# Kernel tuning notes

Measured on AMD Instinct MI355X. Metric: run time of the kernel, lower is better.

Reference implementation:

```python
import jax, jax.numpy as jnp
import numpy as np

LN_EPS = 1e-5

def layer_norm(x, g, b):
    m = x.mean(-1, keepdims=True)
    v = ((x - m) ** 2).mean(-1, keepdims=True)
    return (x - m) / jnp.sqrt(v + LN_EPS) * g + b

def gat_conv(x, src, dst, W, att_src, att_dst, bias, heads, out_ch, concat):
    # PyG GATConv (eval mode, self-loops already included in src/dst).
    N = x.shape[0]
    h = (x @ W).reshape(N, heads, out_ch)                 # [N,H,C]
    a_src = (h * att_src).sum(-1)                          # [N,H]
    a_dst = (h * att_dst).sum(-1)                          # [N,H]
    e = jax.nn.leaky_relu(a_src[src] + a_dst[dst], 0.2)   # [E,H]
    emax = jax.ops.segment_max(e, dst, num_segments=N)    # [N,H]
    ee = jnp.exp(e - emax[dst])
    denom = jax.ops.segment_sum(ee, dst, num_segments=N)  # [N,H]
    alpha = ee / (denom[dst] + 1e-16)                      # [E,H]
    out = jax.ops.segment_sum(alpha[:, :, None] * h[src], dst, num_segments=N)  # [N,H,C]
    out = out.reshape(N, heads * out_ch) if concat else out.mean(axis=1)
    return out + bias

def setup_inputs() -> dict:
    key = jax.random.key(0)
    ks = jax.random.split(key, 32)
    N, G, E = 50000, 405, 300000
    RH, GH, H = 256, 256, 4
    def w(k, shape, fan_in):
        return jax.random.normal(k, shape, dtype=jnp.float32) * (1.0 / np.sqrt(fan_in))
    d = {}
    d["x"] = jax.random.normal(ks[0], (N, G), dtype=jnp.float32)
    d["edge_index"] = jax.random.randint(ks[1], (2, E), 0, N, dtype=jnp.int64)
    # JointEncoder
    d["enc_w1"] = w(ks[2], (G, RH), G); d["enc_b1"] = jnp.zeros(RH)
    d["ln1_g"] = jnp.ones(RH); d["ln1_b"] = jnp.zeros(RH)
    d["enc_w2"] = w(ks[3], (RH, RH), RH); d["enc_b2"] = jnp.zeros(RH)
    d["ln2_g"] = jnp.ones(RH); d["ln2_b"] = jnp.zeros(RH)
    d["w1"] = w(ks[4], (RH, H * GH), RH)
    d["att_src1"] = w(ks[5], (H, GH), GH); d["att_dst1"] = w(ks[6], (H, GH), GH)
    d["bias1"] = jnp.zeros(H * GH)
    d["res1_w"] = w(ks[7], (RH, H * GH), RH); d["res1_b"] = jnp.zeros(H * GH)
    d["w2"] = w(ks[8], (H * GH, 2 * 96), H * GH)
    d["att_src2"] = w(ks[9], (2, 96), 96); d["att_dst2"] = w(ks[10], (2, 96), 96)
    d["bias2"] = jnp.zeros(2 * 96)
    d["res2_w"] = w(ks[11], (H * GH, 2 * 96), H * GH); d["res2_b"] = jnp.zeros(2 * 96)
    d["w3"] = w(ks[12], (192, 128), 192)
    d["att_src3"] = w(ks[13], (1, 128), 128); d["att_dst3"] = w(ks[14], (1, 128), 128)
    d["bias3"] = jnp.zeros(128)
    d["res3_w"] = w(ks[15], (192, 128), 192); d["res3_b"] = jnp.zeros(128)
    # MLP head
    d["mlp_w1"] = w(ks[16], (128, 64), 128); d["mlp_b1"] = jnp.zeros(64)
    d["mlp_w2"] = w(ks[17], (64, 2), 64); d["mlp_b2"] = jnp.zeros(2)
    return d

def reference(x, edge_index, enc_w1, enc_b1, ln1_g, ln1_b, enc_w2, enc_b2, ln2_g, ln2_b,
              w1, att_src1, att_dst1, bias1, res1_w, res1_b,
              w2, att_src2, att_dst2, bias2, res2_w, res2_b,
              w3, att_src3, att_dst3, bias3, res3_w, res3_b,
              mlp_w1, mlp_b1, mlp_w2, mlp_b2):
    N = x.shape[0]
    loop = jnp.arange(N, dtype=edge_index.dtype)
    src = jnp.concatenate([edge_index[0], loop])
    dst = jnp.concatenate([edge_index[1], loop])
    # JointEncoder (eval: dropout is identity)
    h = jax.nn.relu(layer_norm(x @ enc_w1 + enc_b1, ln1_g, ln1_b))
    h = jax.nn.relu(layer_norm(h @ enc_w2 + enc_b2, ln2_g, ln2_b))
    # Block 1
    idn = h
    h = jax.nn.elu(gat_conv(h, src, dst, w1, att_src1, att_dst1, bias1, 4, 256, True))
    h = h + (idn @ res1_w + res1_b)
    # Block 2
    idn = h
    h = jax.nn.elu(gat_conv(h, src, dst, w2, att_src2, att_dst2, bias2, 2, 96, True))
    h = h + (idn @ res2_w + res2_b)
    # Block 3
    idn = h
    h = jax.nn.elu(gat_conv(h, src, dst, w3, att_src3, att_dst3, bias3, 1, 128, False))
    h = h + (idn @ res3_w + res3_b)
    # MLP head
    out = jax.nn.relu(h @ mlp_w1 + mlp_b1) @ mlp_w2 + mlp_b2
    return out
```

## Files before the change

kernel.cpp:

```cpp
#include <hip/hip_runtime.h>
#include <cstddef>

#define LN_EPS 1e-5f

typedef __bf16 bf16x8 __attribute__((ext_vector_type(8)));
typedef float  f32x4  __attribute__((ext_vector_type(4)));

typedef __attribute__((address_space(3))) unsigned int lds_u32;
typedef __attribute__((address_space(1))) unsigned int glb_u32;

__device__ __forceinline__ void gl2lds16(const void* g, void* l) {
    __builtin_amdgcn_global_load_lds((const glb_u32*)g, (lds_u32*)l, 16, 0, 0);
}

__device__ __forceinline__ float b2f(ushort h) {
    return __uint_as_float(((unsigned)h) << 16);
}
__device__ __forceinline__ ushort f2b(float f) {
    unsigned u = __float_as_uint(f);
    return (ushort)((u + 0x7fffu + ((u >> 16) & 1u)) >> 16);
}
__device__ __forceinline__ unsigned pack2(float lo, float hi) {
    return (unsigned)f2b(lo) | ((unsigned)f2b(hi) << 16);
}
__device__ __forceinline__ uint2 pack4(const f32x4 v) {
    return make_uint2(pack2(v[0], v[1]), pack2(v[2], v[3]));
}

__device__ __forceinline__ void xcd_map(int& bx, int& by) {
    int NX = gridDim.x, MBr = gridDim.y;
    int L = blockIdx.y * NX + blockIdx.x;
    int G = NX * 8;
    int g = L / G;
    if (g * 8 + 8 <= MBr) {
        int r = L - g * G;
        by = g * 8 + (r & 7);
        bx = r >> 3;
    } else {
        by = L / NX;
        bx = L - by * NX;
    }
}

__device__ __forceinline__ float wave_allreduce_max(float v) {
    #pragma unroll
    for (int off = 32; off > 0; off >>= 1) v = fmaxf(v, __shfl_xor(v, off, 64));
    return v;
}
__device__ __forceinline__ float wave_allreduce_sum(float v) {
    #pragma unroll
    for (int off = 32; off > 0; off >>= 1) v += __shfl_xor(v, off, 64);
    return v;
}

__device__ __forceinline__ void stage3(const ushort* a0, const ushort* a1, const ushort* b0,
                                       ushort* __restrict__ As, ushort* __restrict__ Bs,
                                       int lb) {
    gl2lds16(a0, As + lb);
    gl2lds16(a1, As + lb + 4096);
    gl2lds16(b0, Bs + lb);
}

__device__ __forceinline__ void mfma_loop256(const ushort* aA0, const ushort* aA1,
                                             const ushort* aB0,
                                             ushort* __restrict__ As, ushort* __restrict__ Bs,
                                             int lb,
                                             int K, int wr, int wc, int cA, int l15,
                                             f32x4 acc[4][4]) {
    const int BUFA = 256 * 32;
    const int BUFB = 128 * 32;
    const int nk = K >> 5;
    stage3(aA0, aA1, aB0, As, Bs, lb);
    int p = 0;
    for (int t = 0; t < nk; t++) {
        asm volatile("s_waitcnt vmcnt(0)" ::: "memory");
        __builtin_amdgcn_s_barrier();
        __builtin_amdgcn_sched_barrier(0);
        int kn = (t + 1) * 32;
        if (kn < K) stage3(aA0 + kn, aA1 + kn, aB0 + kn,
                           As + (p ^ 1) * BUFA, Bs + (p ^ 1) * BUFB, lb);
        const ushort* Ac = As + p * BUFA;
        const ushort* Bc = Bs + p * BUFB;
        bf16x8 af[4], bf[4];
        #pragma unroll
        for (int i = 0; i < 4; i++)
            af[i] = *reinterpret_cast<const bf16x8*>(&Ac[(wr + i * 16 + l15) * 32 + cA]);
        #pragma unroll
        for (int j = 0; j < 4; j++)
            bf[j] = *reinterpret_cast<const bf16x8*>(&Bc[(wc + j * 16 + l15) * 32 + cA]);
        #pragma unroll
        for (int i = 0; i < 4; i++)
            #pragma unroll
            for (int j = 0; j < 4; j++)
                acc[i][j] = __builtin_amdgcn_mfma_f32_16x16x32_bf16(bf[j], af[i], acc[i][j], 0, 0, 0);
        p ^= 1;
    }
    __syncthreads();
}

template<int EPI>
__global__ __launch_bounds__(512, 4) void bgemm(const ushort* __restrict__ A,
                                                const ushort* __restrict__ BT,
                                                const float* __restrict__ bias,
                                                void* __restrict__ out, int ldc,
                                                float* __restrict__ Rf,
                                                float* __restrict__ Sf, int Fs,
                                                int M, int Ncols, int K, int lda) {
    __shared__ ushort As[2][256 * 32];
    __shared__ ushort Bs[2][128 * 32];
    const int tid = threadIdx.x;
    int bx, by; xcd_map(bx, by);
    const int m0 = by * 256, n0 = bx * 128;
    const int w = tid >> 6, lane = tid & 63;
    const int wr = (w >> 1) * 64, wc = (w & 1) * 64;
    const int quad = lane >> 4, l15 = lane & 15;
    const int cA = (quad ^ ((l15 >> 1) & 3)) * 8;
    const int lb = w * 512;

    const int r = tid >> 2, g = ((tid & 3) ^ ((tid >> 3) & 3)) * 8;
    int ga0 = m0 + r;       if (ga0 >= M) ga0 = M - 1;
    int ga1 = m0 + 128 + r; if (ga1 >= M) ga1 = M - 1;
    const ushort* aA0 = A + (size_t)ga0 * lda + g;
    const ushort* aA1 = A + (size_t)ga1 * lda + g;
    const ushort* aB0 = BT + (size_t)(n0 + r) * K + g;

    f32x4 acc[4][4] = {};
    mfma_loop256(aA0, aA1, aB0, As[0], Bs[0], lb, K, wr, wc, cA, l15, acc);

    if (EPI == 4) {
        if (wc == 0) {
            #pragma unroll
            for (int i = 0; i < 4; i++) {
                float o0 = 0.f, o1 = 0.f;
                #pragma unroll
                for (int j = 0; j < 4; j++) {
                    int colbase = j * 16 + quad * 4;
                    float4 bv = *reinterpret_cast<const float4*>(&bias[colbase]);
                    float bb[4] = { bv.x, bv.y, bv.z, bv.w };
                    #pragma unroll
                    for (int rr = 0; rr < 4; rr++) {
                        float vv = fmaxf(acc[i][j][rr] + bb[rr], 0.f);
                        int c = colbase + rr;
                        o0 += vv * Rf[2 * c];
                        o1 += vv * Rf[2 * c + 1];
                    }
                }
                o0 += __shfl_xor(o0, 16, 64); o0 += __shfl_xor(o0, 32, 64);
                o1 += __shfl_xor(o1, 16, 64); o1 += __shfl_xor(o1, 32, 64);
                int row = m0 + wr + i * 16 + l15;
                if (quad == 0 && row < M) {
                    ((float*)out)[(size_t)row * 2]     = o0 + Sf[0];
                    ((float*)out)[(size_t)row * 2 + 1] = o1 + Sf[1];
                }
            }
        }
        return;
    }

    const int twoH = Ncols - 2 * Fs;
    #pragma unroll
    for (int i = 0; i < 4; i++) {
        int row = m0 + wr + i * 16 + l15;
        if (row >= M) continue;
        #pragma unroll
        for (int j = 0; j < 4; j++) {
            int colbase = n0 + wc + j * 16 + quad * 4;
            if (EPI == 0) {
                f32x4 v = acc[i][j];
                if (bias) {
                    float4 bv = *reinterpret_cast<const float4*>(&bias[colbase]);
                    v[0] += bv.x; v[1] += bv.y; v[2] += bv.z; v[3] += bv.w;
                }
                *reinterpret_cast<f32x4*>(&((float*)out)[(size_t)row * ldc + colbase]) = v;
            } else if (EPI == 5) {
                if (colbase + 3 < Fs) {
                    *reinterpret_cast<uint2*>(&((ushort*)out)[(size_t)row * Fs + colbase]) = pack4(acc[i][j]);
                } else if (colbase >= Fs && colbase + 3 < 2 * Fs) {
                    *reinterpret_cast<f32x4*>(&Rf[(size_t)row * Fs + (colbase - Fs)]) = acc[i][j];
                } else {
                    #pragma unroll
                    for (int rr = 0; rr < 4; rr++) {
                        int col = colbase + rr;
                        if (col < 2 * Fs || col >= Ncols) continue;
                        Sf[(size_t)row * twoH + (col - 2 * Fs)] = acc[i][j][rr];
                    }
                }
            }
        }
    }
}

__global__ __launch_bounds__(512, 4) void bgemm_b1(const ushort* __restrict__ accb,
                                                   const ushort* __restrict__ w1T,
                                                   const ushort* __restrict__ h1b,
                                                   const ushort* __restrict__ res1T,
                                                   const float* __restrict__ bias1,
                                                   const float* __restrict__ res1b,
                                                   ushort* __restrict__ H2b, int M) {
    __shared__ ushort As[2][256 * 32];
    __shared__ ushort Bs[2][128 * 32];
    const int tid = threadIdx.x;
    int bx, by; xcd_map(bx, by);
    const int m0 = by * 256, n0 = bx * 128;
    const int h = n0 >> 8;
    const int w = tid >> 6, lane = tid & 63;
    const int wr = (w >> 1) * 64, wc = (w & 1) * 64;
    const int quad = lane >> 4, l15 = lane & 15;
    const int cA = (quad ^ ((l15 >> 1) & 3)) * 8;
    const int lb = w * 512;

    const int r = tid >> 2, g = ((tid & 3) ^ ((tid >> 3) & 3)) * 8;
    int ga0 = m0 + r;       if (ga0 >= M) ga0 = M - 1;
    int ga1 = m0 + 128 + r; if (ga1 >= M) ga1 = M - 1;

    f32x4 acc[4][4] = {};

    mfma_loop256(accb + (size_t)ga0 * 1024 + h * 256 + g,
                 accb + (size_t)ga1 * 1024 + h * 256 + g,
                 w1T + (size_t)(n0 + r) * 256 + g,
                 As[0], Bs[0], lb, 256, wr, wc, cA, l15, acc);

    #pragma unroll
    for (int i = 0; i < 4; i++) {
        #pragma unroll
        for (int j = 0; j < 4; j++) {
            int colbase = n0 + wc + j * 16 + quad * 4;
            float4 bv = *reinterpret_cast<const float4*>(&bias1[colbase]);
            float4 rv = *reinterpret_cast<const float4*>(&res1b[colbase]);
            float bb[4] = { bv.x, bv.y, bv.z, bv.w };
            float rr[4] = { rv.x, rv.y, rv.z, rv.w };
            #pragma unroll
            for (int q = 0; q < 4; q++) {
                float t = acc[i][j][q] + bb[q];
                t = t > 0.f ? t : (__expf(t) - 1.f);
                acc[i][j][q] = t + rr[q];
            }
        }
    }

    mfma_loop256(h1b + (size_t)ga0 * 256 + g,
                 h1b + (size_t)ga1 * 256 + g,
                 res1T + (size_t)(n0 + r) * 256 + g,
                 As[0], Bs[0], lb, 256, wr, wc, cA, l15, acc);

    #pragma unroll
    for (int i = 0; i < 4; i++) {
        int row = m0 + wr + i * 16 + l15;
        if (row >= M) continue;
        #pragma unroll
        for (int j = 0; j < 4; j++) {
            int colbase = n0 + wc + j * 16 + quad * 4;
            *reinterpret_cast<uint2*>(&H2b[(size_t)row * 1024 + colbase]) = pack4(acc[i][j]);
        }
    }
}

__global__ void conv_pad_x_kernel(const float* __restrict__ x, ushort* __restrict__ xb, int N) {
    int t = blockIdx.x * 256 + threadIdx.x;
    if (t >= N * 448) return;
    int n = t / 448, k = t - n * 448;
    xb[t] = f2b(k < 405 ? x[(size_t)n * 405 + k] : 0.f);
}

__device__ __forceinline__ void prep_seg(int t, const float* src, ushort* dst,
                                         int K, int Nreal, int Kpad, int ldsrc) {
    int n = t / Kpad, k = t - n * Kpad;
    float v = (k < K && n < Nreal) ? src[(size_t)k * ldsrc + n] : 0.f;
    dst[t] = f2b(v);
}

__global__ void prep_all_kernel(const float* __restrict__ enc_w1, const float* __restrict__ enc_w2,
                                const float* __restrict__ w1, const float* __restrict__ res1_w,
                                const float* __restrict__ w2, const float* __restrict__ res2_w,
                                const float* __restrict__ w3, const float* __restrict__ res3_w,
                                const float* __restrict__ mlp_w1,
                                ushort* __restrict__ enc_w1T, ushort* __restrict__ enc_w2T,
                                ushort* __restrict__ w1T, ushort* __restrict__ res1T,
                                ushort* __restrict__ Bcat2T, ushort* __restrict__ Bcat3T,
                                ushort* __restrict__ mlpw1T) {
    int t = blockIdx.x * 256 + threadIdx.x;
    const int c0 = 114688;
    const int c1 = c0 + 65536;
    const int c2 = c1 + 262144;
    const int c3 = c2 + 262144;
    const int c4 = c3 + 196608;
    const int c5 = c4 + 196608;
    const int c6 = c5 + 126976;
    const int c7 = c6 + 24576;
    const int c8 = c7 + 24576;
    const int c9 = c8 + 24192;
    const int c10 = c9 + 16384;
    if (t < c0)      prep_seg(t,        enc_w1, enc_w1T, 405, 256, 448, 256);
    else if (t < c1) prep_seg(t - c0,   enc_w2, enc_w2T, 256, 256, 256, 256);
    else if (t < c2) prep_seg(t - c1,   w1,     w1T,     256, 1024, 256, 1024);
    else if (t < c3) prep_seg(t - c2,   res1_w, res1T,   256, 1024, 256, 1024);
    else if (t < c4) prep_seg(t - c3,   w2,     Bcat2T,  1024, 192, 1024, 192);
    else if (t < c5) prep_seg(t - c4,   res2_w, Bcat2T + (size_t)192 * 1024, 1024, 192, 1024, 192);
    else if (t < c6) Bcat2T[(size_t)388 * 1024 + (t - c5)] = 0;
    else if (t < c7) prep_seg(t - c6,   w3,     Bcat3T,  192, 128, 192, 128);
    else if (t < c8) prep_seg(t - c7,   res3_w, Bcat3T + (size_t)128 * 192, 192, 128, 192, 128);
    else if (t < c9) Bcat3T[(size_t)258 * 192 + (t - c8)] = 0;
    else if (t < c10) prep_seg(t - c9,  mlp_w1, mlpw1T,  128, 64, 128, 64);
}

template<int H>
__global__ __launch_bounds__(256) void ln_relu_w_kernel(const float* __restrict__ x,
                                                        const float* __restrict__ g,
                                                        const float* __restrict__ b,
                                                        const float* __restrict__ qs,
                                                        const float* __restrict__ qd,
                                                        ushort* __restrict__ out,
                                                        float* __restrict__ a_s,
                                                        float* __restrict__ a_d,
                                                        int N) {
    const int lane = threadIdx.x & 63;
    int wid = blockIdx.x * 4 + (threadIdx.x >> 6);
    const int nw = gridDim.x * 4;
    const int c4 = lane * 4;

    f32x4 gv = *reinterpret_cast<const f32x4*>(&g[c4]);
    f32x4 bv = *reinterpret_cast<const f32x4*>(&b[c4]);
    f32x4 qsv[H > 0 ? H : 1], qdv[H > 0 ? H : 1];
    if (H > 0) {
        #pragma unroll
        for (int hh = 0; hh < H; hh++) {
            qsv[hh] = *reinterpret_cast<const f32x4*>(&qs[hh * 256 + c4]);
            qdv[hh] = *reinterpret_cast<const f32x4*>(&qd[hh * 256 + c4]);
        }
    }

    for (int row = wid; row < N; row += nw) {
        f32x4 v = *reinterpret_cast<const f32x4*>(&x[(size_t)row * 256 + c4]);
        float s  = v[0] + v[1] + v[2] + v[3];
        float s2 = v[0] * v[0] + v[1] * v[1] + v[2] * v[2] + v[3] * v[3];
        #pragma unroll
        for (int off = 32; off > 0; off >>= 1) {
            s  += __shfl_xor(s,  off, 64);
            s2 += __shfl_xor(s2, off, 64);
        }
        float m   = s * (1.f / 256.f);
        float var = s2 * (1.f / 256.f) - m * m;
        float rs  = rsqrtf(var + LN_EPS);
        f32x4 o;
        #pragma unroll
        for (int k = 0; k < 4; k++) o[k] = fmaxf((v[k] - m) * rs * gv[k] + bv[k], 0.f);
        *reinterpret_cast<uint2*>(&out[(size_t)row * 256 + c4]) =
            make_uint2(pack2(o[0], o[1]), pack2(o[2], o[3]));
        if (H > 0) {
            float sc[H > 0 ? 2 * H : 1];
            #pragma unroll
            for (int hh = 0; hh < H; hh++) {
                sc[hh]     = o[0] * qsv[hh][0] + o[1] * qsv[hh][1] + o[2] * qsv[hh][2] + o[3] * qsv[hh][3];
                sc[H + hh] = o[0] * qdv[hh][0] + o[1] * qdv[hh][1] + o[2] * qdv[hh][2] + o[3] * qdv[hh][3];
            }
            #pragma unroll
            for (int off = 32; off > 0; off >>= 1)
                #pragma unroll
                for (int k = 0; k < 2 * H; k++) sc[k] += __shfl_xor(sc[k], off, 64);
            if (lane == 0) {
                #pragma unroll
                for (int k = 0; k < H; k++) a_s[(size_t)row * H + k] = sc[k];
            } else if (lane == 1) {
                #pragma unroll
                for (int k = 0; k < H; k++) a_d[(size_t)row * H + k] = sc[H + k];
            }
        }
    }
}

__global__ void fold_att_kernel(const float* __restrict__ W,
                                const float* __restrict__ att_s,
                                const float* __restrict__ att_d,
                                float* __restrict__ qs, float* __restrict__ qd,
                                int Cin, int Cout, int H) {
    int t = blockIdx.x * blockDim.x + threadIdx.x;
    if (t >= H * Cin) return;
    int h = t / Cin, k = t - h * Cin;
    const float* wrow = W + (size_t)k * (H * Cout) + (size_t)h * Cout;
    const float* as = att_s + (size_t)h * Cout;
    const float* ad = att_d + (size_t)h * Cout;
    float ss = 0.f, sd = 0.f;
    for (int c = 0; c < Cout; c++) { float wv = wrow[c]; ss += wv * as[c]; sd += wv * ad[c]; }
    qs[t] = ss;
    qd[t] = sd;
}

__global__ void fold_att_b16_kernel(const float* __restrict__ W,
                                    const float* __restrict__ att_s,
                                    const float* __restrict__ att_d,
                                    ushort* __restrict__ qs_b, ushort* __restrict__ qd_b,
                                    int Cin, int Cout, int H) {
    int t = blockIdx.x * blockDim.x + threadIdx.x;
    if (t >= H * Cin) return;
    int h = t / Cin, k = t - h * Cin;
    const float* wrow = W + (size_t)k * (H * Cout) + (size_t)h * Cout;
    const float* as = att_s + (size_t)h * Cout;
    const float* ad = att_d + (size_t)h * Cout;
    float ss = 0.f, sd = 0.f;
    for (int c = 0; c < Cout; c++) { float wv = wrow[c]; ss += wv * as[c]; sd += wv * ad[c]; }
    qs_b[t] = f2b(ss);
    qd_b[t] = f2b(sd);
}

__device__ __forceinline__ void edge_sd(const int* ei, int e, int E, int& s, int& d) {
    if (e < E) { s = ei[e]; d = ei[E + e]; } else { s = d = e - E; }
}

__global__ void deg_kernel(const int* __restrict__ ei, int* __restrict__ deg, int E, int Et) {
    int e = blockIdx.x * blockDim.x + threadIdx.x;
    if (e >= Et) return;
    int s, d; edge_sd(ei, e, E, s, d);
    atomicAdd(&deg[d], 1);
}

__global__ __launch_bounds__(256) void scan1_kernel(const int* __restrict__ deg,
                                                    int* __restrict__ incl,
                                                    int* __restrict__ part, int N) {
    __shared__ int sd[256];
    int t = threadIdx.x;
    int i = blockIdx.x * 256 + t;
    int v = (i < N) ? deg[i] : 0;
    sd[t] = v; __syncthreads();
    #pragma unroll
    for (int o = 1; o < 256; o <<= 1) {
        int x = (t >= o) ? sd[t - o] : 0;
        __syncthreads();
        sd[t] += x;
        __syncthreads();
    }
    if (i < N) incl[i] = sd[t];
    if (t == 255) part[blockIdx.x] = sd[255];
}

__global__ __launch_bounds__(256) void scan2_kernel(int* __restrict__ part, int nb) {
    __shared__ int sd[256];
    int t = threadIdx.x;
    int v = (t < nb) ? part[t] : 0;
    sd[t] = v; __syncthreads();
    #pragma unroll
    for (int o = 1; o < 256; o <<= 1) {
        int x = (t >= o) ? sd[t - o] : 0;
        __syncthreads();
        sd[t] += x;
        __syncthreads();
    }
    if (t < nb) part[t] = sd[t];
}

__global__ void scan3_kernel(const int* __restrict__ incl, const int* __restrict__ deg,
                             const int* __restrict__ part, int* __restrict__ row_ptr, int N) {
    int i = blockIdx.x * blockDim.x + threadIdx.x;
    if (i >= N) return;
    int off = (blockIdx.x > 0) ? part[blockIdx.x - 1] : 0;
    row_ptr[i] = incl[i] - deg[i] + off;
}

__global__ void fill_kernel(const int* __restrict__ ei, const int* __restrict__ row_ptr,
                            int* __restrict__ cur, int* __restrict__ csr_src, int E, int Et) {
    int e = blockIdx.x * blockDim.x + threadIdx.x;
    if (e >= Et) return;
    int s, d; edge_sd(ei, e, E, s, d);
    int pos = row_ptr[d] + atomicAdd(&cur[d], 1);
    csr_src[pos] = s;
}

#define ACAP 256

__global__ __launch_bounds__(128) void aggr_b1_fused_kernel(const int* __restrict__ row_ptr,
                                                            const int* __restrict__ deg,
                                                            const int* __restrict__ csr_src,
                                                            const float* __restrict__ a_s,
                                                            const float* __restrict__ a_d,
                                                            const ushort* __restrict__ h1b,
                                                            ushort* __restrict__ accb) {
    __shared__ float alf[ACAP][4];
    __shared__ float sstat[8];
    int d = blockIdx.x, t = threadIdx.x;
    int base = row_ptr[d], dg = deg[d];
    float4 ad = *reinterpret_cast<const float4*>(&a_d[(size_t)d * 4]);
    if (t < 64) {
        float m0 = -1e30f, m1 = -1e30f, m2 = -1e30f, m3 = -1e30f;
        for (int j = t; j < dg; j += 64) {
            int s = csr_src[base + j];
            float4 sv = *reinterpret_cast<const float4*>(&a_s[(size_t)s * 4]);
            float c0 = sv.x + ad.x; c0 = c0 > 0.f ? c0 : 0.2f * c0; m0 = fmaxf(m0, c0);
            float c1 = sv.y + ad.y; c1 = c1 > 0.f ? c1 : 0.2f * c1; m1 = fmaxf(m1, c1);
            float c2 = sv.z + ad.z; c2 = c2 > 0.f ? c2 : 0.2f * c2; m2 = fmaxf(m2, c2);
            float c3 = sv.w + ad.w; c3 = c3 > 0.f ? c3 : 0.2f * c3; m3 = fmaxf(m3, c3);
        }
        m0 = wave_allreduce_max(m0); m1 = wave_allreduce_max(m1);
        m2 = wave_allreduce_max(m2); m3 = wave_allreduce_max(m3);
        float s0 = 0.f, s1 = 0.f, s2 = 0.f, s3 = 0.f;
        for (int j = t; j < dg; j += 64) {
            int s = csr_src[base + j];
            float4 sv = *reinterpret_cast<const float4*>(&a_s[(size_t)s * 4]);
            float c0 = sv.x + ad.x; c0 = c0 > 0.f ? c0 : 0.2f * c0; float e0 = __expf(c0 - m0); s0 += e0;
            float c1 = sv.y + ad.y; c1 = c1 > 0.f ? c1 : 0.2f * c1; float e1 = __expf(c1 - m1); s1 += e1;
            float c2 = sv.z + ad.z; c2 = c2 > 0.f ? c2 : 0.2f * c2; float e2 = __expf(c2 - m2); s2 += e2;
            float c3 = sv.w + ad.w; c3 = c3 > 0.f ? c3 : 0.2f * c3; float e3 = __expf(c3 - m3); s3 += e3;
            if (j < ACAP) { alf[j][0] = e0; alf[j][1] = e1; alf[j][2] = e2; alf[j][3] = e3; }
        }
        s0 = wave_allreduce_sum(s0); s1 = wave_allreduce_sum(s1);
        s2 = wave_allreduce_sum(s2); s3 = wave_allreduce_sum(s3);
        if (t == 0) {
            sstat[0] = m0; sstat[1] = m1; sstat[2] = m2; sstat[3] = m3;
            sstat[4] = 1.f / (s0 + 1e-16f); sstat[5] = 1.f / (s1 + 1e-16f);
            sstat[6] = 1.f / (s2 + 1e-16f); sstat[7] = 1.f / (s3 + 1e-16f);
        }
    }
    __syncthreads();
    float r0 = sstat[4], r1 = sstat[5], r2 = sstat[6], r3 = sstat[7];
    float a00 = 0, a01 = 0, a10 = 0, a11 = 0, a20 = 0, a21 = 0, a30 = 0, a31 = 0;
    for (int j = 0; j < dg; j++) {
        int s = csr_src[base + j];
        float al0, al1, al2, al3;
        if (j < ACAP) {
            al0 = alf[j][0] * r0; al1 = alf[j][1] * r1;
            al2 = alf[j][2] * r2; al3 = alf[j][3] * r3;
        } else {
            float4 sv = *reinterpret_cast<const float4*>(&a_s[(size_t)s * 4]);
            float c0 = sv.x + ad.x; c0 = c0 > 0.f ? c0 : 0.2f * c0; al0 = __expf(c0 - sstat[0]) * r0;
            float c1 = sv.y + ad.y; c1 = c1 > 0.f ? c1 : 0.2f * c1; al1 = __expf(c1 - sstat[1]) * r1;
            float c2 = sv.z + ad.z; c2 = c2 > 0.f ? c2 : 0.2f * c2; al2 = __expf(c2 - sstat[2]) * r2;
            float c3 = sv.w + ad.w; c3 = c3 > 0.f ? c3 : 0.2f * c3; al3 = __expf(c3 - sstat[3]) * r3;
        }
        unsigned v = reinterpret_cast<const unsigned*>(h1b + (size_t)s * 256)[t];
        float lo = b2f((ushort)(v & 0xffff)), hi = b2f((ushort)(v >> 16));
        a00 += al0 * lo; a01 += al0 * hi;
        a10 += al1 * lo; a11 += al1 * hi;
        a20 += al2 * lo; a21 += al2 * hi;
        a30 += al3 * lo; a31 += al3 * hi;
    }
    unsigned* o = reinterpret_cast<unsigned*>(accb + (size_t)d * 1024);
    o[t]       = pack2(a00, a01);
    o[t + 128] = pack2(a10, a11);
    o[t + 256] = pack2(a20, a21);
    o[t + 384] = pack2(a30, a31);
}

template<int H, int C, int F, int NT>
__global__ __launch_bounds__(NT) void aggr_comb_fused_kernel(const int* __restrict__ row_ptr,
                                                             const int* __restrict__ deg,
                                                             const int* __restrict__ csr_src,
                                                             const float* __restrict__ as,
                                                             const ushort* __restrict__ g,
                                                             const float* __restrict__ Rf,
                                                             const float* __restrict__ gb,
                                                             const float* __restrict__ rb,
                                                             ushort* __restrict__ outb) {
    __shared__ float alf[ACAP][H];
    __shared__ float sstat[2 * H];
    int d = blockIdx.x;
    int t = threadIdx.x;
    int base = row_ptr[d], dg = deg[d];
    if (t < 64) {
        float ad[H], mx[H];
        #pragma unroll
        for (int h = 0; h < H; h++) { ad[h] = as[(size_t)d * 2 * H + H + h]; mx[h] = -1e30f; }
        for (int j = t; j < dg; j += 64) {
            int s = csr_src[base + j];
            #pragma unroll
            for (int h = 0; h < H; h++) {
                float c = as[(size_t)s * 2 * H + h] + ad[h];
                c = c > 0.f ? c : 0.2f * c;
                mx[h] = fmaxf(mx[h], c);
            }
        }
        #pragma unroll
        for (int h = 0; h < H; h++) mx[h] = wave_allreduce_max(mx[h]);
        float sm[H];
        #pragma unroll
        for (int h = 0; h < H; h++) sm[h] = 0.f;
        for (int j = t; j < dg; j += 64) {
            int s = csr_src[base + j];
            #pragma unroll
            for (int h = 0; h < H; h++) {
                float c = as[(size_t)s * 2 * H + h] + ad[h];
                c = c > 0.f ? c : 0.2f * c;
                float e = __expf(c - mx[h]);
                sm[h] += e;
                if (j < ACAP) alf[j][h] = e;
            }
        }
        #pragma unroll
        for (int h = 0; h < H; h++) sm[h] = wave_allreduce_sum(sm[h]);
        if (t == 0) {
            #pragma unroll
            for (int h = 0; h < H; h++) { sstat[h] = mx[h]; sstat[H + h] = 1.f / (sm[h] + 1e-16f); }
        }
    }
    __syncthreads();
    int hd = (2 * t) / C;
    float mxv = sstat[hd], rdv = sstat[H + hd];
    float adv = as[(size_t)d * 2 * H + H + hd];
    float lo = 0.f, hi = 0.f;
    for (int j = 0; j < dg; j++) {
        int s = csr_src[base + j];
        float al;
        if (j < ACAP) al = alf[j][hd] * rdv;
        else {
            float c = as[(size_t)s * 2 * H + hd] + adv;
            c = c > 0.f ? c : 0.2f * c;
            al = __expf(c - mxv) * rdv;
        }
        unsigned v = reinterpret_cast<const unsigned*>(g + (size_t)s * F)[t];
        lo += al * b2f((ushort)(v & 0xffff));
        hi += al * b2f((ushort)(v >> 16));
    }
    int c0 = 2 * t, c1 = 2 * t + 1;
    float o0 = lo + gb[c0]; o0 = o0 > 0.f ? o0 : (__expf(o0) - 1.f);
    float o1 = hi + gb[c1]; o1 = o1 > 0.f ? o1 : (__expf(o1) - 1.f);
    o0 += Rf[(size_t)d * F + c0] + rb[c0];
    o1 += Rf[(size_t)d * F + c1] + rb[c1];
    reinterpret_cast<unsigned*>(outb)[(size_t)d * (F / 2) + t] = pack2(o0, o1);
}

extern "C" void kernel_launch(void* const* d_in, const int* in_sizes, int n_in,
                              void* d_out, int out_size, void* d_ws, size_t ws_size,
                              hipStream_t stream) {
    const float* x        = (const float*)d_in[0];
    const int*   ei       = (const int*)d_in[1];
    const float* enc_w1   = (const float*)d_in[2];
    const float* enc_b1   = (const float*)d_in[3];
    const float* ln1_g    = (const float*)d_in[4];
    const float* ln1_b    = (const float*)d_in[5];
    const float* enc_w2   = (const float*)d_in[6];
    const float* enc_b2   = (const float*)d_in[7];
    const float* ln2_g    = (const float*)d_in[8];
    const float* ln2_b    = (const float*)d_in[9];
    const float* w1       = (const float*)d_in[10];
    const float* att_src1 = (const float*)d_in[11];
    const float* att_dst1 = (const float*)d_in[12];
    const float* bias1    = (const float*)d_in[13];
    const float* res1_w   = (const float*)d_in[14];
    const float* res1_b   = (const float*)d_in[15];
    const float* w2       = (const float*)d_in[16];
    const float* att_src2 = (const float*)d_in[17];
    const float* att_dst2 = (const float*)d_in[18];
    const float* bias2    = (const float*)d_in[19];
    const float* res2_b_  = (const float*)d_in[21];
    const float* res2_w   = (const float*)d_in[20];
    const float* w3       = (const float*)d_in[22];
    const float* att_src3 = (const float*)d_in[23];
    const float* att_dst3 = (const float*)d_in[24];
    const float* bias3    = (const float*)d_in[25];
    const float* res3_w   = (const float*)d_in[26];
    const float* res3_b   = (const float*)d_in[27];
    const float* mlp_w1   = (const float*)d_in[28];
    const float* mlp_b1   = (const float*)d_in[29];
    const float* mlp_w2   = (const float*)d_in[30];
    const float* mlp_b2   = (const float*)d_in[31];
    const float* res2_b   = res2_b_;

    const int N  = in_sizes[0] / 405;
    const int E  = in_sizes[1] / 2;
    const int Et = E + N;
    const int NB = (N + 255) / 256;

    char* p = (char*)d_ws;
    char* R0 = p;
    char* R1 = R0 + (size_t)N * 896;
    char* R2 = R1 + (size_t)N * 512;
    char* R3 = R2 + (size_t)N * 512;
    char* R4 = R3 + (size_t)N * 2048;
    char* T  = R4 + (size_t)N * 2048;

    ushort* xb   = (ushort*)R0;
    ushort* H3b  = (ushort*)R0;
    ushort* h0b  = (ushort*)R1;
    ushort* G2b  = (ushort*)R1;
    ushort* h1b  = (ushort*)R2;
    ushort* G3b  = (ushort*)R2;
    ushort* H4b  = (ushort*)(R2 + (size_t)N * 256);
    float*  F1   = (float*)R3;
    ushort* H2b  = (ushort*)R3;
    ushort* accb = (ushort*)R4;
    float*  Rf   = (float*)R4;

    float* a_s   = (float*)T;                         T += (size_t)N * 4 * 4;
    float* a_d   = (float*)T;                         T += (size_t)N * 4 * 4;
    float* qs    = (float*)T;                         T += 2048 * 4;
    float* qd    = (float*)T;                         T += 2048 * 4;
    int* deg     = (int*)T;                           T += (size_t)N * 4;
    int* cur     = (int*)T;                           T += (size_t)N * 4;
    int* row_ptr = (int*)T;                           T += (size_t)N * 4;
    int* incl    = (int*)T;                           T += (size_t)N * 4;
    int* part    = (int*)T;                           T += 256 * 4;
    int* csr_src = (int*)T;                           T += (size_t)Et * 4;
    ushort* enc_w1T = (ushort*)T;                     T += (size_t)256 * 448 * 2;
    ushort* enc_w2T = (ushort*)T;                     T += (size_t)256 * 256 * 2;
    ushort* w1T     = (ushort*)T;                     T += (size_t)1024 * 256 * 2;
    ushort* res1T   = (ushort*)T;                     T += (size_t)1024 * 256 * 2;
    ushort* Bcat2T  = (ushort*)T;                     T += (size_t)512 * 1024 * 2;
    ushort* Bcat3T  = (ushort*)T;                     T += (size_t)384 * 192 * 2;
    ushort* mlpw1T  = (ushort*)T;                     T += (size_t)128 * 128 * 2;

    auto cdiv = [](int a, int b) { return (a + b - 1) / b; };
    const int MBr = cdiv(N, 256);

    hipMemsetAsync(deg, 0, (size_t)N * 8, stream);
    deg_kernel<<<cdiv(Et, 256), 256, 0, stream>>>(ei, deg, E, Et);
    scan1_kernel<<<NB, 256, 0, stream>>>(deg, incl, part, N);
    scan2_kernel<<<1, 256, 0, stream>>>(part, NB);
    scan3_kernel<<<NB, 256, 0, stream>>>(incl, deg, part, row_ptr, N);
    fill_kernel<<<cdiv(Et, 256), 256, 0, stream>>>(ei, row_ptr, cur, csr_src, E, Et);

    prep_all_kernel<<<cdiv(1314432, 256), 256, 0, stream>>>(
        enc_w1, enc_w2, w1, res1_w, w2, res2_w, w3, res3_w, mlp_w1,
        enc_w1T, enc_w2T, w1T, res1T, Bcat2T, Bcat3T, mlpw1T);

    fold_att_kernel<<<cdiv(4 * 256, 256), 256, 0, stream>>>(w1, att_src1, att_dst1, qs, qd, 256, 256, 4);

    conv_pad_x_kernel<<<cdiv(N * 448, 256), 256, 0, stream>>>(x, xb, N);
    bgemm<0><<<dim3(2, MBr), 512, 0, stream>>>(xb, enc_w1T, enc_b1, F1, 256, nullptr, nullptr, 0, N, 256, 448, 448);
    ln_relu_w_kernel<0><<<1024, 256, 0, stream>>>(F1, ln1_g, ln1_b, nullptr, nullptr, h0b, nullptr, nullptr, N);
    bgemm<0><<<dim3(2, MBr), 512, 0, stream>>>(h0b, enc_w2T, enc_b2, F1, 256, nullptr, nullptr, 0, N, 256, 256, 256);
    ln_relu_w_kernel<4><<<1024, 256, 0, stream>>>(F1, ln2_g, ln2_b, qs, qd, h1b, a_s, a_d, N);

    aggr_b1_fused_kernel<<<N, 128, 0, stream>>>(row_ptr, deg, csr_src, a_s, a_d, h1b, accb);
    bgemm_b1<<<dim3(8, MBr), 512, 0, stream>>>(accb, w1T, h1b, res1T, bias1, res1_b, H2b, N);

    {
        fold_att_b16_kernel<<<cdiv(2 * 1024, 256), 256, 0, stream>>>(w2, att_src2, att_dst2,
            Bcat2T + (size_t)384 * 1024, Bcat2T + (size_t)386 * 1024, 1024, 96, 2);
        bgemm<5><<<dim3(4, MBr), 512, 0, stream>>>(H2b, Bcat2T, nullptr, G2b, 0, Rf, a_s, 192, N, 388, 1024, 1024);
        aggr_comb_fused_kernel<2, 96, 192, 96><<<N, 96, 0, stream>>>(row_ptr, deg, csr_src, a_s,
                                                                     G2b, Rf, bias2, res2_b, H3b);
    }

    {
        fold_att_b16_kernel<<<1, 256, 0, stream>>>(w3, att_src3, att_dst3,
            Bcat3T + (size_t)256 * 192, Bcat3T + (size_t)257 * 192, 192, 128, 1);
        bgemm<5><<<dim3(3, MBr), 512, 0, stream>>>(H3b, Bcat3T, nullptr, G3b, 0, Rf, a_s, 128, N, 258, 192, 192);
        aggr_comb_fused_kernel<1, 128, 128, 64><<<N, 64, 0, stream>>>(row_ptr, deg, csr_src, a_s,
                                                                      G3b, Rf, bias3, res3_b, H4b);
    }

    bgemm<4><<<dim3(1, MBr), 512, 0, stream>>>(H4b, mlpw1T, mlp_b1, d_out, 2,
                                               (float*)mlp_w2, (float*)mlp_b2, 0, N, 64, 128, 128);
}
```

Before: 803.1 us.

## Fuse attention folding into prep kernel, process two rows per wave, unroll aggregation

Merges the three attention-vector folding kernels into the weight-prep kernel, using wave-parallel reductions instead of serial per-thread loops, which removes launches and long serial dot products. The layer-norm kernel now handles two rows per wave iteration and its grid doubles, raising memory-level parallelism. The edge aggregation loops are unrolled by two so two gathered rows are loaded before their accumulations, hiding gather latency. It costs more registers and a more complex prep kernel.

After: 724.3 us. 9.8% less time.

```diff
diff --git a/kernel.cpp b/kernel.cpp
--- a/kernel.cpp
+++ b/kernel.cpp
@@ -262,6 +262,7 @@
     xb[t] = f2b(k < 405 ? x[(size_t)n * 405 + k] : 0.f);
 }
 
+#define PREP_PB 5135
 __device__ __forceinline__ void prep_seg(int t, const float* src, ushort* dst,
                                          int K, int Nreal, int Kpad, int ldsrc) {
     int n = t / Kpad, k = t - n * Kpad;
@@ -269,38 +270,93 @@
     dst[t] = f2b(v);
 }
 
-__global__ void prep_all_kernel(const float* __restrict__ enc_w1, const float* __restrict__ enc_w2,
-                                const float* __restrict__ w1, const float* __restrict__ res1_w,
-                                const float* __restrict__ w2, const float* __restrict__ res2_w,
-                                const float* __restrict__ w3, const float* __restrict__ res3_w,
-                                const float* __restrict__ mlp_w1,
-                                ushort* __restrict__ enc_w1T, ushort* __restrict__ enc_w2T,
-                                ushort* __restrict__ w1T, ushort* __restrict__ res1T,
-                                ushort* __restrict__ Bcat2T, ushort* __restrict__ Bcat3T,
-                                ushort* __restrict__ mlpw1T) {
-    int t = blockIdx.x * 256 + threadIdx.x;
-    const int c0 = 114688;
-    const int c1 = c0 + 65536;
-    const int c2 = c1 + 262144;
-    const int c3 = c2 + 262144;
-    const int c4 = c3 + 196608;
-    const int c5 = c4 + 196608;
-    const int c6 = c5 + 126976;
-    const int c7 = c6 + 24576;
-    const int c8 = c7 + 24576;
-    const int c9 = c8 + 24192;
-    const int c10 = c9 + 16384;
-    if (t < c0)      prep_seg(t,        enc_w1, enc_w1T, 405, 256, 448, 256);
-    else if (t < c1) prep_seg(t - c0,   enc_w2, enc_w2T, 256, 256, 256, 256);
-    else if (t < c2) prep_seg(t - c1,   w1,     w1T,     256, 1024, 256, 1024);
-    else if (t < c3) prep_seg(t - c2,   res1_w, res1T,   256, 1024, 256, 1024);
-    else if (t < c4) prep_seg(t - c3,   w2,     Bcat2T,  1024, 192, 1024, 192);
-    else if (t < c5) prep_seg(t - c4,   res2_w, Bcat2T + (size_t)192 * 1024, 1024, 192, 1024, 192);
-    else if (t < c6) Bcat2T[(size_t)388 * 1024 + (t - c5)] = 0;
-    else if (t < c7) prep_seg(t - c6,   w3,     Bcat3T,  192, 128, 192, 128);
-    else if (t < c8) prep_seg(t - c7,   res3_w, Bcat3T + (size_t)128 * 192, 192, 128, 192, 128);
-    else if (t < c9) Bcat3T[(size_t)258 * 192 + (t - c8)] = 0;
-    else if (t < c10) prep_seg(t - c9,  mlp_w1, mlpw1T,  128, 64, 128, 64);
+__global__ void prep_fold_kernel(const float* __restrict__ enc_w1, const float* __restrict__ enc_w2,
+                                 const float* __restrict__ w1, const float* __restrict__ res1_w,
+                                 const float* __restrict__ w2, const float* __restrict__ res2_w,
+                                 const float* __restrict__ w3, const float* __restrict__ res3_w,
+                                 const float* __restrict__ mlp_w1,
+                                 const float* __restrict__ att_s1, const float* __restrict__ att_d1,
+                                 const float* __restrict__ att_s2, const float* __restrict__ att_d2,
+                                 const float* __restrict__ att_s3, const float* __restrict__ att_d3,
+                                 ushort* __restrict__ enc_w1T, ushort* __restrict__ enc_w2T,
+                                 ushort* __restrict__ w1T, ushort* __restrict__ res1T,
+                                 ushort* __restrict__ Bcat2T, ushort* __restrict__ Bcat3T,
+                                 ushort* __restrict__ mlpw1T,
+                                 float* __restrict__ qs, float* __restrict__ qd) {
+    int blk = blockIdx.x;
+    if (blk < PREP_PB) {
+        int t = blk * 256 + threadIdx.x;
+        const int c0 = 114688;
+        const int c1 = c0 + 65536;
+        const int c2 = c1 + 262144;
+        const int c3 = c2 + 262144;
+        const int c4 = c3 + 196608;
+        const int c5 = c4 + 196608;
+        const int c6 = c5 + 126976;
+        const int c7 = c6 + 24576;
+        const int c8 = c7 + 24576;
+        const int c9 = c8 + 24192;
+        const int c10 = c9 + 16384;
+        if (t < c0)      prep_seg(t,        enc_w1, enc_w1T, 405, 256, 448, 256);
+        else if (t < c1) prep_seg(t - c0,   enc_w2, enc_w2T, 256, 256, 256, 256);
+        else if (t < c2) prep_seg(t - c1,   w1,     w1T,     256, 1024, 256, 1024);
+        else if (t < c3) prep_seg(t - c2,   res1_w, res1T,   256, 1024, 256, 1024);
+        else if (t < c4) prep_seg(t - c3,   w2,     Bcat2T,  1024, 192, 1024, 192);
+        else if (t < c5) prep_seg(t - c4,   res2_w, Bcat2T + (size_t)192 * 1024, 1024, 192, 1024, 192);
+        else if (t < c6) Bcat2T[(size_t)388 * 1024 + (t - c5)] = 0;
+        else if (t < c7) prep_seg(t - c6,   w3,     Bcat3T,  192, 128, 192, 128);
+        else if (t < c8) prep_seg(t - c7,   res3_w, Bcat3T + (size_t)128 * 192, 192, 128, 192, 128);
+        else if (t < c9) Bcat3T[(size_t)258 * 192 + (t - c8)] = 0;
+        else if (t < c10) prep_seg(t - c9,  mlp_w1, mlpw1T,  128, 64, 128, 64);
+        return;
+    }
+    int fw = (blk - PREP_PB) * 4 + (threadIdx.x >> 6);
+    int lane = threadIdx.x & 63;
+    if (fw < 1024) {
+        int h = fw >> 8, k = fw & 255;
+        const float* wrow = w1 + (size_t)k * 1024 + h * 256;
+        f32x4 wv = *reinterpret_cast<const f32x4*>(&wrow[lane * 4]);
+        f32x4 as = *reinterpret_cast<const f32x4*>(&att_s1[h * 256 + lane * 4]);
+        f32x4 ad = *reinterpret_cast<const f32x4*>(&att_d1[h * 256 + lane * 4]);
+        float ss = wv[0] * as[0] + wv[1] * as[1] + wv[2] * as[2] + wv[3] * as[3];
+        float sd = wv[0] * ad[0] + wv[1] * ad[1] + wv[2] * ad[2] + wv[3] * ad[3];
+        ss = wave_allreduce_sum(ss);
+        sd = wave_allreduce_sum(sd);
+        if (lane == 0) { qs[fw] = ss; qd[fw] = sd; }
+    } else if (fw < 1024 + 2048) {
+        int t = fw - 1024;
+        int h = t >> 10, k = t & 1023;
+        const float* wrow = w2 + (size_t)k * 192 + h * 96;
+        const float* as = att_s2 + h * 96;
+        const float* ad = att_d2 + h * 96;
+        float w0 = wrow[lane];
+        float ss = w0 * as[lane], sd = w0 * ad[lane];
+        if (lane < 32) {
+            float w1v = wrow[64 + lane];
+            ss += w1v * as[64 + lane];
+            sd += w1v * ad[64 + lane];
+        }
+        ss = wave_allreduce_sum(ss);
+        sd = wave_allreduce_sum(sd);
+        if (lane == 0) {
+            Bcat2T[(size_t)384 * 1024 + t] = f2b(ss);
+            Bcat2T[(size_t)386 * 1024 + t] = f2b(sd);
+        }
+    } else {
+        int t = fw - 3072;
+        if (t < 192) {
+            const float* wrow = w3 + (size_t)t * 128;
+            float w0 = wrow[lane], w1v = wrow[64 + lane];
+            float ss = w0 * att_s3[lane] + w1v * att_s3[64 + lane];
+            float sd = w0 * att_d3[lane] + w1v * att_d3[64 + lane];
+            ss = wave_allreduce_sum(ss);
+            sd = wave_allreduce_sum(sd);
+            if (lane == 0) {
+                Bcat3T[(size_t)256 * 192 + t] = f2b(ss);
+                Bcat3T[(size_t)257 * 192 + t] = f2b(sd);
+            }
+        }
+    }
 }
 
 template<int H>
@@ -329,77 +385,65 @@
         }
     }
 
-    for (int row = wid; row < N; row += nw) {
-        f32x4 v = *reinterpret_cast<const f32x4*>(&x[(size_t)row * 256 + c4]);
-        float s  = v[0] + v[1] + v[2] + v[3];
-        float s2 = v[0] * v[0] + v[1] * v[1] + v[2] * v[2] + v[3] * v[3];
+    for (int r0 = wid * 2; r0 < N; r0 += 2 * nw) {
+        int r1 = r0 + 1;
+        bool has1 = r1 < N;
+        f32x4 va = *reinterpret_cast<const f32x4*>(&x[(size_t)r0 * 256 + c4]);
+        f32x4 vb = has1 ? *reinterpret_cast<const f32x4*>(&x[(size_t)r1 * 256 + c4]) : va;
+        float sa  = va[0] + va[1] + va[2] + va[3];
+        float s2a = va[0] * va[0] + va[1] * va[1] + va[2] * va[2] + va[3] * va[3];
+        float sb  = vb[0] + vb[1] + vb[2] + vb[3];
+        float s2b = vb[0] * vb[0] + vb[1] * vb[1] + vb[2] * vb[2] + vb[3] * vb[3];
         #pragma unroll
         for (int off = 32; off > 0; off >>= 1) {
-            s  += __shfl_xor(s,  off, 64);
-            s2 += __shfl_xor(s2, off, 64);
-        }
-        float m   = s * (1.f / 256.f);
-        float var = s2 * (1.f / 256.f) - m * m;
-        float rs  = rsqrtf(var + LN_EPS);
-        f32x4 o;
-        #pragma unroll
-        for (int k = 0; k < 4; k++) o[k] = fmaxf((v[k] - m) * rs * gv[k] + bv[k], 0.f);
-        *reinterpret_cast<uint2*>(&out[(size_t)row * 256 + c4]) =
-            make_uint2(pack2(o[0], o[1]), pack2(o[2], o[3]));
+            sa  += __shfl_xor(sa,  off, 64);
+            sb  += __shfl_xor(sb,  off, 64);
+            s2a += __shfl_xor(s2a, off, 64);
+            s2b += __shfl_xor(s2b, off, 64);
+        }
+        float ma  = sa * (1.f / 256.f);
+        float mb  = sb * (1.f / 256.f);
+        float rsa = rsqrtf(s2a * (1.f / 256.f) - ma * ma + LN_EPS);
+        float rsb = rsqrtf(s2b * (1.f / 256.f) - mb * mb + LN_EPS);
+        f32x4 oa, ob;
+        #pragma unroll
+        for (int k = 0; k < 4; k++) {
+            oa[k] = fmaxf((va[k] - ma) * rsa * gv[k] + bv[k], 0.f);
+            ob[k] = fmaxf((vb[k] - mb) * rsb * gv[k] + bv[k], 0.f);
+        }
+        *reinterpret_cast<uint2*>(&out[(size_t)r0 * 256 + c4]) =
+            make_uint2(pack2(oa[0], oa[1]), pack2(oa[2], oa[3]));
+        if (has1)
+            *reinterpret_cast<uint2*>(&out[(size_t)r1 * 256 + c4]) =
+                make_uint2(pack2(ob[0], ob[1]), pack2(ob[2], ob[3]));
         if (H > 0) {
-            float sc[H > 0 ? 2 * H : 1];
+            float sc[H > 0 ? 4 * H : 1];
             #pragma unroll
             for (int hh = 0; hh < H; hh++) {
-                sc[hh]     = o[0] * qsv[hh][0] + o[1] * qsv[hh][1] + o[2] * qsv[hh][2] + o[3] * qsv[hh][3];
-                sc[H + hh] = o[0] * qdv[hh][0] + o[1] * qdv[hh][1] + o[2] * qdv[hh][2] + o[3] * qdv[hh][3];
+                sc[hh]           = oa[0] * qsv[hh][0] + oa[1] * qsv[hh][1] + oa[2] * qsv[hh][2] + oa[3] * qsv[hh][3];
+                sc[H + hh]       = oa[0] * qdv[hh][0] + oa[1] * qdv[hh][1] + oa[2] * qdv[hh][2] + oa[3] * qdv[hh][3];
+                sc[2 * H + hh]   = ob[0] * qsv[hh][0] + ob[1] * qsv[hh][1] + ob[2] * qsv[hh][2] + ob[3] * qsv[hh][3];
+                sc[3 * H + hh]   = ob[0] * qdv[hh][0] + ob[1] * qdv[hh][1] + ob[2] * qdv[hh][2] + ob[3] * qdv[hh][3];
             }
             #pragma unroll
             for (int off = 32; off > 0; off >>= 1)
                 #pragma unroll
-                for (int k = 0; k < 2 * H; k++) sc[k] += __shfl_xor(sc[k], off, 64);
+                for (int k = 0; k < 4 * H; k++) sc[k] += __shfl_xor(sc[k], off, 64);
             if (lane == 0) {
                 #pragma unroll
-                for (int k = 0; k < H; k++) a_s[(size_t)row * H + k] = sc[k];
+                for (int k = 0; k < H; k++) a_s[(size_t)r0 * H + k] = sc[k];
+                if (has1)
+                    #pragma unroll
+                    for (int k = 0; k < H; k++) a_s[(size_t)r1 * H + k] = sc[2 * H + k];
             } else if (lane == 1) {
                 #pragma unroll
-                for (int k = 0; k < H; k++) a_d[(size_t)row * H + k] = sc[H + k];
+                for (int k = 0; k < H; k++) a_d[(size_t)r0 * H + k] = sc[H + k];
+                if (has1)
+                    #pragma unroll
+                    for (int k = 0; k < H; k++) a_d[(size_t)r1 * H + k] = sc[3 * H + k];
             }
         }
     }
-}
-
-__global__ void fold_att_kernel(const float* __restrict__ W,
-                                const float* __restrict__ att_s,
-                                const float* __restrict__ att_d,
-                                float* __restrict__ qs, float* __restrict__ qd,
-                                int Cin, int Cout, int H) {
-    int t = blockIdx.x * blockDim.x + threadIdx.x;
-    if (t >= H * Cin) return;
-    int h = t / Cin, k = t - h * Cin;
-    const float* wrow = W + (size_t)k * (H * Cout) + (size_t)h * Cout;
-    const float* as = att_s + (size_t)h * Cout;
-    const float* ad = att_d + (size_t)h * Cout;
-    float ss = 0.f, sd = 0.f;
-    for (int c = 0; c < Cout; c++) { float wv = wrow[c]; ss += wv * as[c]; sd += wv * ad[c]; }
-    qs[t] = ss;
-    qd[t] = sd;
-}
-
-__global__ void fold_att_b16_kernel(const float* __restrict__ W,
-                                    const float* __restrict__ att_s,
-                                    const float* __restrict__ att_d,
-                                    ushort* __restrict__ qs_b, ushort* __restrict__ qd_b,
-                                    int Cin, int Cout, int H) {
-    int t = blockIdx.x * blockDim.x + threadIdx.x;
-    if (t >= H * Cin) return;
-    int h = t / Cin, k = t - h * Cin;
-    const float* wrow = W + (size_t)k * (H * Cout) + (size_t)h * Cout;
-    const float* as = att_s + (size_t)h * Cout;
-    const float* ad = att_d + (size_t)h * Cout;
-    float ss = 0.f, sd = 0.f;
-    for (int c = 0; c < Cout; c++) { float wv = wrow[c]; ss += wv * as[c]; sd += wv * ad[c]; }
-    qs_b[t] = f2b(ss);
-    qd_b[t] = f2b(sd);
 }
 
 __device__ __forceinline__ void edge_sd(const int* ei, int e, int E, int& s, int& d) {
@@ -511,9 +555,8 @@
     __syncthreads();
     float r0 = sstat[4], r1 = sstat[5], r2 = sstat[6], r3 = sstat[7];
     float a00 = 0, a01 = 0, a10 = 0, a11 = 0, a20 = 0, a21 = 0, a30 = 0, a31 = 0;
-    for (int j = 0; j < dg; j++) {
-        int s = csr_src[base + j];
-        float al0, al1, al2, al3;
+
+    auto alpha4 = [&](int j, int s, float& al0, float& al1, float& al2, float& al3) {
         if (j < ACAP) {
             al0 = alf[j][0] * r0; al1 = alf[j][1] * r1;
             al2 = alf[j][2] * r2; al3 = alf[j][3] * r3;
@@ -524,12 +567,32 @@
             float c2 = sv.z + ad.z; c2 = c2 > 0.f ? c2 : 0.2f * c2; al2 = __expf(c2 - sstat[2]) * r2;
             float c3 = sv.w + ad.w; c3 = c3 > 0.f ? c3 : 0.2f * c3; al3 = __expf(c3 - sstat[3]) * r3;
         }
-        unsigned v = reinterpret_cast<const unsigned*>(h1b + (size_t)s * 256)[t];
-        float lo = b2f((ushort)(v & 0xffff)), hi = b2f((ushort)(v >> 16));
-        a00 += al0 * lo; a01 += al0 * hi;
-        a10 += al1 * lo; a11 += al1 * hi;
-        a20 += al2 * lo; a21 += al2 * hi;
-        a30 += al3 * lo; a31 += al3 * hi;
+    };
+    int j = 0;
+    for (; j + 2 <= dg; j += 2) {
+        int s0i = csr_src[base + j], s1i = csr_src[base + j + 1];
+        unsigned v0 = reinterpret_cast<const unsigned*>(h1b + (size_t)s0i * 256)[t];
+        unsigned v1 = reinterpret_cast<const unsigned*>(h1b + (size_t)s1i * 256)[t];
+        float x0, x1, x2, x3, y0, y1, y2, y3;
+        alpha4(j, s0i, x0, x1, x2, x3);
+        alpha4(j + 1, s1i, y0, y1, y2, y3);
+        float lo0 = b2f((ushort)(v0 & 0xffff)), hi0 = b2f((ushort)(v0 >> 16));
+        float lo1 = b2f((ushort)(v1 & 0xffff)), hi1 = b2f((ushort)(v1 >> 16));
+        a00 += x0 * lo0 + y0 * lo1; a01 += x0 * hi0 + y0 * hi1;
+        a10 += x1 * lo0 + y1 * lo1; a11 += x1 * hi0 + y1 * hi1;
+        a20 += x2 * lo0 + y2 * lo1; a21 += x2 * hi0 + y2 * hi1;
+        a30 += x3 * lo0 + y3 * lo1; a31 += x3 * hi0 + y3 * hi1;
+    }
+    if (j < dg) {
+        int s0i = csr_src[base + j];
+        unsigned v0 = reinterpret_cast<const unsigned*>(h1b + (size_t)s0i * 256)[t];
+        float x0, x1, x2, x3;
+        alpha4(j, s0i, x0, x1, x2, x3);
+        float lo0 = b2f((ushort)(v0 & 0xffff)), hi0 = b2f((ushort)(v0 >> 16));
+        a00 += x0 * lo0; a01 += x0 * hi0;
+        a10 += x1 * lo0; a11 += x1 * hi0;
+        a20 += x2 * lo0; a21 += x2 * hi0;
+        a30 += x3 * lo0; a31 += x3 * hi0;
     }
     unsigned* o = reinterpret_cast<unsigned*>(accb + (size_t)d * 1024);
     o[t]       = pack2(a00, a01);
@@ -594,18 +657,27 @@
     float mxv = sstat[hd], rdv = sstat[H + hd];
     float adv = as[(size_t)d * 2 * H + H + hd];
     float lo = 0.f, hi = 0.f;
-    for (int j = 0; j < dg; j++) {
-        int s = csr_src[base + j];
-        float al;
-        if (j < ACAP) al = alf[j][hd] * rdv;
-        else {
-            float c = as[(size_t)s * 2 * H + hd] + adv;
-            c = c > 0.f ? c : 0.2f * c;
-            al = __expf(c - mxv) * rdv;
-        }
-        unsigned v = reinterpret_cast<const unsigned*>(g + (size_t)s * F)[t];
-        lo += al * b2f((ushort)(v & 0xffff));
-        hi += al * b2f((ushort)(v >> 16));
+    auto alpha1 = [&](int j, int s) -> float {
+        if (j < ACAP) return alf[j][hd] * rdv;
+        float c = as[(size_t)s * 2 * H + hd] + adv;
+        c = c > 0.f ? c : 0.2f * c;
+        return __expf(c - mxv) * rdv;
+    };
+    int j = 0;
+    for (; j + 2 <= dg; j += 2) {
+        int s0 = csr_src[base + j], s1 = csr_src[base + j + 1];
+        unsigned v0 = reinterpret_cast<const unsigned*>(g + (size_t)s0 * F)[t];
+        unsigned v1 = reinterpret_cast<const unsigned*>(g + (size_t)s1 * F)[t];
+        float al0 = alpha1(j, s0), al1 = alpha1(j + 1, s1);
+        lo += al0 * b2f((ushort)(v0 & 0xffff)) + al1 * b2f((ushort)(v1 & 0xffff));
+        hi += al0 * b2f((ushort)(v0 >> 16))    + al1 * b2f((ushort)(v1 >> 16));
+    }
+    if (j < dg) {
+        int s0 = csr_src[base + j];
+        unsigned v0 = reinterpret_cast<const unsigned*>(g + (size_t)s0 * F)[t];
+        float al0 = alpha1(j, s0);
+        lo += al0 * b2f((ushort)(v0 & 0xffff));
+        hi += al0 * b2f((ushort)(v0 >> 16));
     }
     int c0 = 2 * t, c1 = 2 * t + 1;
     float o0 = lo + gb[c0]; o0 = o0 > 0.f ? o0 : (__expf(o0) - 1.f);
@@ -638,8 +710,8 @@
     const float* att_src2 = (const float*)d_in[17];
     const float* att_dst2 = (const float*)d_in[18];
     const float* bias2    = (const float*)d_in[19];
-    const float* res2_b_  = (const float*)d_in[21];
     const float* res2_w   = (const float*)d_in[20];
+    const float* res2_b   = (const float*)d_in[21];
     const float* w3       = (const float*)d_in[22];
     const float* att_src3 = (const float*)d_in[23];
     const float* att_dst3 = (const float*)d_in[24];
@@ -650,7 +722,6 @@
     const float* mlp_b1   = (const float*)d_in[29];
     const float* mlp_w2   = (const float*)d_in[30];
     const float* mlp_b2   = (const float*)d_in[31];
-    const float* res2_b   = res2_b_;
 
     const int N  = in_sizes[0] / 405;
     const int E  = in_sizes[1] / 2;
@@ -698,39 +769,34 @@
     auto cdiv = [](int a, int b) { return (a + b - 1) / b; };
     const int MBr = cdiv(N, 256);
 
-    hipMemsetAsync(deg, 0, (size_t)N * 8, stream);
+    (void)hipMemsetAsync(deg, 0, (size_t)N * 8, stream);
     deg_kernel<<<cdiv(Et, 256), 256, 0, stream>>>(ei, deg, E, Et);
     scan1_kernel<<<NB, 256, 0, stream>>>(deg, incl, part, N);
     scan2_kernel<<<1, 256, 0, stream>>>(part, NB);
     scan3_kernel<<<NB, 256, 0, stream>>>(incl, deg, part, row_ptr, N);
     fill_kernel<<<cdiv(Et, 256), 256, 0, stream>>>(ei, row_ptr, cur, csr_src, E, Et);
 
-    prep_all_kernel<<<cdiv(1314432, 256), 256, 0, stream>>>(
+    prep_fold_kernel<<<PREP_PB + 816, 256, 0, stream>>>(
         enc_w1, enc_w2, w1, res1_w, w2, res2_w, w3, res3_w, mlp_w1,
-        enc_w1T, enc_w2T, w1T, res1T, Bcat2T, Bcat3T, mlpw1T);
-
-    fold_att_kernel<<<cdiv(4 * 256, 256), 256, 0, stream>>>(w1, att_src1, att_dst1, qs, qd, 256, 256, 4);
+        att_src1, att_dst1, att_src2, att_dst2, att_src3, att_dst3,
+        enc_w1T, enc_w2T, w1T, res1T, Bcat2T, Bcat3T, mlpw1T, qs, qd);
 
     conv_pad_x_kernel<<<cdiv(N * 448, 256), 256, 0, stream>>>(x, xb, N);
     bgemm<0><<<dim3(2, MBr), 512, 0, stream>>>(xb, enc_w1T, enc_b1, F1, 256, nullptr, nullptr, 0, N, 256, 448, 448);
-    ln_relu_w_kernel<0><<<1024, 256, 0, stream>>>(F1, ln1_g, ln1_b, nullptr, nullptr, h0b, nullptr, nullptr, N);
+    ln_relu_w_kernel<0><<<2048, 256, 0, stream>>>(F1, ln1_g, ln1_b, nullptr, nullptr, h0b, nullptr, nullptr, N);
     bgemm<0><<<dim3(2, MBr), 512, 0, stream>>>(h0b, enc_w2T, enc_b2, F1, 256, nullptr, nullptr, 0, N, 256, 256, 256);
-    ln_relu_w_kernel<4><<<1024, 256, 0, stream>>>(F1, ln2_g, ln2_b, qs, qd, h1b, a_s, a_d, N);
+    ln_relu_w_kernel<4><<<2048, 256, 0, stream>>>(F1, ln2_g, ln2_b, qs, qd, h1b, a_s, a_d, N);
 
     aggr_b1_fused_kernel<<<N, 128, 0, stream>>>(row_ptr, deg, csr_src, a_s, a_d, h1b, accb);
     bgemm_b1<<<dim3(8, MBr), 512, 0, stream>>>(accb, w1T, h1b, res1T, bias1, res1_b, H2b, N);
 
     {
-        fold_att_b16_kernel<<<cdiv(2 * 1024, 256), 256, 0, stream>>>(w2, att_src2, att_dst2,
-            Bcat2T + (size_t)384 * 1024, Bcat2T + (size_t)386 * 1024, 1024, 96, 2);
         bgemm<5><<<dim3(4, MBr), 512, 0, stream>>>(H2b, Bcat2T, nullptr, G2b, 0, Rf, a_s, 192, N, 388, 1024, 1024);
         aggr_comb_fused_kernel<2, 96, 192, 96><<<N, 96, 0, stream>>>(row_ptr, deg, csr_src, a_s,
                                                                      G2b, Rf, bias2, res2_b, H3b);
     }
 
     {
-        fold_att_b16_kernel<<<1, 256, 0, stream>>>(w3, att_src3, att_dst3,
-            Bcat3T + (size_t)256 * 192, Bcat3T + (size_t)257 * 192, 192, 128, 1);
         bgemm<5><<<dim3(3, MBr), 512, 0, stream>>>(H3b, Bcat3T, nullptr, G3b, 0, Rf, a_s, 128, N, 258, 192, 192);
         aggr_comb_fused_kernel<1, 128, 128, 64><<<N, 64, 0, stream>>>(row_ptr, deg, csr_src, a_s,
                                                                       G3b, Rf, bias3, res3_b, H4b);
```
